# Performance work log

Measured on AMD Instinct MI355X. Metric: run time of the kernel, lower is better.

The kernel has to match this reference:

```python
import jax, jax.numpy as jnp
import numpy as np

B, N, K = 16, 2048, 20
EPS = 1e-5
SLOPE = 0.2  # LeakyReLU negative slope


def _lrelu(x):
    return jnp.where(x >= 0, x, SLOPE * x)


def _bn(x, g, b, axes):
    # BatchNorm in training mode (batch statistics), channel-last layout
    m = x.mean(axes, keepdims=True)
    v = x.var(axes, keepdims=True)
    return (x - m) * jax.lax.rsqrt(v + EPS) * g + b


def _graph_features(pts, k):
    # pts: [B, N, C] -> edge features [B, N, k, 2C] = concat(x_j - x_i, x_i)
    xx = jnp.sum(pts * pts, axis=-1)                       # [B, N]
    inner = jnp.einsum('bnc,bmc->bnm', pts, pts)           # [B, N, N]
    neg_d = 2.0 * inner - xx[:, :, None] - xx[:, None, :]  # -||x_i - x_j||^2
    _, idx = jax.lax.top_k(neg_d, k)                       # [B, N, k]
    xj = jax.vmap(lambda p, i: p[i])(pts, idx)             # [B, N, k, C]
    xi = pts[:, :, None, :]                                # [B, N, 1, C]
    return jnp.concatenate([xj - xi, jnp.broadcast_to(xi, xj.shape)], axis=-1)


def _forward(x, conv_w, conv_g, conv_b, w1, b1, g1, bt1, w2, b2, g2, bt2,
             w3, b3, g3, bt3, w4, b4, w5, b5):
    feat = _graph_features(x, K)                           # [B, N, K, 6]
    # 1x1 Conv2d (bias=False) + BN2d + LeakyReLU, then max over neighbors
    h = jnp.einsum('bnkc,oc->bnko', feat, conv_w)          # [B, N, K, 64]
    h = _lrelu(_bn(h, conv_g, conv_b, (0, 1, 2)))
    h = h.max(axis=2)                                      # [B, N, 64]
    # DBR blocks: Linear + BN1d + LeakyReLU over points
    h = _lrelu(_bn(h @ w1 + b1, g1, bt1, (0, 1)))          # [B, N, 64]
    h = _lrelu(_bn(h @ w2 + b2, g2, bt2, (0, 1)))          # [B, N, 128]
    h = _lrelu(_bn(h @ w3 + b3, g3, bt3, (0, 1)))          # [B, N, 128]
    h = h.max(axis=1)                                      # MaxChannel -> [B, 128]
    h = _lrelu(h @ w4 + b4)                                # DbR -> [B, 512]
    return h @ w5 + b5                                     # [B, 2*Z_DIM=256]


def setup_inputs() -> dict:
    key = jax.random.key(0)
    ks = jax.random.split(key, 8)
    rn = lambda k, s, sc: (jax.random.normal(k, s, jnp.float32) * sc)
    return {
        'x': jax.random.normal(ks[0], (B, N, 3), jnp.float32),
        'conv_w': rn(ks[1], (64, 6), 0.3),
        'conv_g': jnp.ones(64, jnp.float32), 'conv_b': jnp.zeros(64, jnp.float32),
        'w1': rn(ks[2], (64, 64), 0.1), 'b1': jnp.zeros(64, jnp.float32),
        'g1': jnp.ones(64, jnp.float32), 'bt1': jnp.zeros(64, jnp.float32),
        'w2': rn(ks[3], (64, 128), 0.1), 'b2': jnp.zeros(128, jnp.float32),
        'g2': jnp.ones(128, jnp.float32), 'bt2': jnp.zeros(128, jnp.float32),
        'w3': rn(ks[4], (128, 128), 0.1), 'b3': jnp.zeros(128, jnp.float32),
        'g3': jnp.ones(128, jnp.float32), 'bt3': jnp.zeros(128, jnp.float32),
        'w4': rn(ks[5], (128, 512), 0.05), 'b4': jnp.zeros(512, jnp.float32),
        'w5': rn(ks[6], (512, 256), 0.05), 'b5': jnp.zeros(256, jnp.float32),
    }


def reference(x, conv_w, conv_g, conv_b, w1, b1, g1, bt1, w2, b2, g2, bt2,
              w3, b3, g3, bt3, w4, b4, w5, b5):
    return _forward(x, conv_w, conv_g, conv_b, w1, b1, g1, bt1, w2, b2, g2, bt2,
                    w3, b3, g3, bt3, w4, b4, w5, b5)
```

## Files before the change

### kernel.cpp

```cpp
#include <hip/hip_runtime.h>
#include <math.h>

#define NB   16
#define NPTS 2048
#define KNBR 20
#define NROWS (NB*NPTS)
#define CONV_M ((double)(NB)*(double)(NPTS)*(double)(KNBR))
#define ROW_M  ((double)NROWS)
#define BN_EPS 1e-5
#define LSLOPE 0.2f

__device__ __forceinline__ float lrelu(float v) { return v >= 0.f ? v : LSLOPE * v; }

__device__ __forceinline__ float4 stage4(float px, float py, float pz)
{
    return make_float4(px + px, py + py, pz + pz,
                       -fmaf(px, px, fmaf(py, py, pz * pz)));
}

__device__ __forceinline__ float dist_eval(float4 q, float4 c)
{
    float t = fmaf(c.x, q.x, fmaf(c.y, q.y, fmaf(c.z, q.z, q.w)));
    return t + c.w;
}

__device__ __forceinline__ void pair_insert_sorted(float (&bestv)[KNBR], float t0, float t1)
{
#pragma unroll
    for (int j = 0; j < KNBR; ++j) {
        float bj = bestv[j];
        float nb  = fmaxf(bj, t0);
        float nt0 = __builtin_amdgcn_fmed3f(bj, t0, t1);
        float nt1 = fminf(bj, t1);
        bestv[j] = nb;
        t0 = nt0; t1 = nt1;
    }
}

__global__ __launch_bounds__(256) void knn_feat_kernel(const float* __restrict__ x,
        const float* __restrict__ conv_w,
        float* __restrict__ maxh, float* __restrict__ minh, double* __restrict__ S)
{
    __shared__ float4 pts[NPTS];
    __shared__ unsigned short idxl[32][KNBR];
    __shared__ float  featw[4][KNBR][6];
    __shared__ double sred[4][27];
    __shared__ float  tbuf[32];
    const int b  = blockIdx.x >> 6;
    const int qg = blockIdx.x & 63;
    const float* xb = x + (size_t)b * NPTS * 3;
    for (int i = threadIdx.x; i < NPTS; i += 256)
        pts[i] = stage4(xb[i*3+0], xb[i*3+1], xb[i*3+2]);
    __syncthreads();

    {
        const int qi = threadIdx.x >> 3;
        const int c  = threadIdx.x & 7;
        const int n  = qg * 32 + qi;
        const float4 qc = pts[n];
        const float4 q = make_float4(0.5f*qc.x, 0.5f*qc.y, 0.5f*qc.z, qc.w);
        const int cbase = c * 256;
        const int rot   = (37 * c) & 255;
        float bestv[KNBR];
#pragma unroll
        for (int j = 0; j < KNBR; ++j) bestv[j] = -__builtin_inff();
        for (int m = 0; m < 64; m += 2) {
            const int j0 = (m + rot) & 255;
            const int j1 = (j0 + 1) & 255;
            float d0 = dist_eval(q, pts[cbase + j0]);
            float d1 = dist_eval(q, pts[cbase + j1]);
            pair_insert_sorted(bestv, fmaxf(d0, d1), fminf(d0, d1));
        }
        float L = bestv[KNBR-1];
        L = fmaxf(L, __shfl_xor(L, 1));
        L = fmaxf(L, __shfl_xor(L, 2));
        L = fmaxf(L, __shfl_xor(L, 4));
#pragma unroll
        for (int j = 0; j < KNBR; ++j) bestv[j] = fmaxf(bestv[j], L);
        float thresh = bestv[KNBR-1];
        float r0 = -__builtin_inff(), r1 = r0, r2 = r0, r3 = r0;
        int rc = 0;
        for (int m = 64; m < 256; m += 2) {
            const int j0 = (m + rot) & 255;
            const int j1 = (j0 + 1) & 255;
            float d0 = dist_eval(q, pts[cbase + j0]);
            float d1 = dist_eval(q, pts[cbase + j1]);
            bool h0 = d0 > thresh;
            r3 = h0 ? r2 : r3; r2 = h0 ? r1 : r2; r1 = h0 ? r0 : r1; r0 = h0 ? d0 : r0;
            rc += h0 ? 1 : 0;
            bool h1 = d1 > thresh;
            r3 = h1 ? r2 : r3; r2 = h1 ? r1 : r2; r1 = h1 ? r0 : r1; r0 = h1 ? d1 : r0;
            rc += h1 ? 1 : 0;
            if (__any(rc >= 3)) {
                pair_insert_sorted(bestv, fmaxf(r0, r1), fminf(r0, r1));
                pair_insert_sorted(bestv, fmaxf(r2, r3), fminf(r2, r3));
                r0 = r1 = r2 = r3 = -__builtin_inff();
                rc = 0;
                thresh = bestv[KNBR-1];
            }
        }
        pair_insert_sorted(bestv, fmaxf(r0, r1), fminf(r0, r1));
        pair_insert_sorted(bestv, fmaxf(r2, r3), fminf(r2, r3));
#pragma unroll
        for (int lev = 1; lev <= 4; lev <<= 1) {
            float orig[KNBR];
#pragma unroll
            for (int j = 0; j < KNBR; ++j) orig[j] = bestv[j];
            for (int i = 0; i < KNBR; i += 2) {
                float nb0 = __shfl_xor(orig[i],   lev);
                float nb1 = __shfl_xor(orig[i+1], lev);
                if (!__any(nb0 > bestv[KNBR-1])) break;
                pair_insert_sorted(bestv, nb0, nb1);
            }
        }
        if (c == 0) tbuf[qi] = bestv[KNBR-1];
    }
    __syncthreads();

    const int wv = threadIdx.x >> 6, lane = threadIdx.x & 63;
    const unsigned long long below = (1ull << lane) - 1ull;
    for (int qi2 = 0; qi2 < 8; ++qi2) {
        const int p = wv * 8 + qi2;
        const int n = qg * 32 + p;
        const float4 qc = pts[n];
        const float4 q = make_float4(0.5f*qc.x, 0.5f*qc.y, 0.5f*qc.z, qc.w);
        const float th = tbuf[p];
        int cnt = 0;
        for (int it = 0; it < 32; ++it) {
            float d = dist_eval(q, pts[it*64 + lane]);
            const bool hit = (d >= th);
            unsigned long long mask = __ballot(hit);
            int pos = cnt + __popcll(mask & below);
            if (hit && pos < KNBR)
                idxl[p][pos] = (unsigned short)(it*64 + lane);
            cnt += __popcll(mask);
        }
    }
    __syncthreads();

    float cw[6];
#pragma unroll
    for (int c = 0; c < 6; ++c) cw[c] = conv_w[lane*6 + c];
    int pa_ = 0, pb_ = 0;
    if (lane >= 6 && lane < 27) {
        int t = lane - 6, a = 0;
        while (t >= 6 - a) { t -= 6 - a; ++a; }
        pa_ = a; pb_ = a + t;
    }
    double acc = 0.0;
    for (int i = 0; i < 8; ++i) {
        const int p = wv * 8 + i;
        const int nn = qg * 32 + p;
        const size_t bp = (size_t)b * NPTS + nn;
        const float4 Ci = pts[nn];
        const float xi0 = 0.5f*Ci.x, xi1 = 0.5f*Ci.y, xi2 = 0.5f*Ci.z;
        float f0=0,f1=0,f2=0,f3=0,f4=0,f5=0;
        if (lane < KNBR) {
            const float4 Cj = pts[idxl[p][lane]];
            f0 = 0.5f*(Cj.x - Ci.x);
            f1 = 0.5f*(Cj.y - Ci.y);
            f2 = 0.5f*(Cj.z - Ci.z);
            f3 = xi0; f4 = xi1; f5 = xi2;
        }
        __syncthreads();
        if (lane < KNBR) {
            featw[wv][lane][0]=f0; featw[wv][lane][1]=f1; featw[wv][lane][2]=f2;
            featw[wv][lane][3]=f3; featw[wv][lane][4]=f4; featw[wv][lane][5]=f5;
        }
        __syncthreads();
        float vmax = -__builtin_inff(), vmin = __builtin_inff();
#pragma unroll
        for (int k = 0; k < KNBR; ++k) {
            float h = featw[wv][k][0] * cw[0];
            h = fmaf(featw[wv][k][1], cw[1], h);
            h = fmaf(featw[wv][k][2], cw[2], h);
            h = fmaf(featw[wv][k][3], cw[3], h);
            h = fmaf(featw[wv][k][4], cw[4], h);
            h = fmaf(featw[wv][k][5], cw[5], h);
            vmax = fmaxf(vmax, h); vmin = fminf(vmin, h);
        }
        maxh[bp*64 + lane] = vmax;
        minh[bp*64 + lane] = vmin;
        if (lane < 6) {
            double s = 0;
#pragma unroll
            for (int k = 0; k < KNBR; ++k) s += (double)featw[wv][k][lane];
            acc += s;
        } else if (lane < 27) {
            double s = 0;
#pragma unroll
            for (int k = 0; k < KNBR; ++k)
                s += (double)featw[wv][k][pa_] * (double)featw[wv][k][pb_];
            acc += s;
        }
    }
    if (lane < 27) sred[wv][lane] = acc;
    __syncthreads();
    if (threadIdx.x < 27) {
        double tot = sred[0][threadIdx.x] + sred[1][threadIdx.x]
                   + sred[2][threadIdx.x] + sred[3][threadIdx.x];
        atomicAdd(&S[threadIdx.x], tot);
    }
}

template<int K, int N, bool SEL, bool POOLOUT, bool STATS0>
__global__ __launch_bounds__(256) void mlp_gemm(const float* __restrict__ A,
        const float* __restrict__ A2,
        const double* __restrict__ st_a, const double* __restrict__ st_b,
        const float* __restrict__ st_g, const float* __restrict__ st_bt,
        const float* __restrict__ cwm,
        const float* __restrict__ W, const float* __restrict__ bias,
        float* __restrict__ Y, double* __restrict__ sum, double* __restrict__ sq,
        float* __restrict__ pmax_g, float* __restrict__ pmin_g)
{
    constexpr int CPT = N / 16;
    __shared__ float As[64 * 64];
    __shared__ float Ws[64 * N];
    __shared__ __align__(16) float s_scale[K], s_shift[K];
    const int tid = threadIdx.x;
    if (tid < K) {
        const int o = tid;
        if (STATS0) {
            double w[6];
#pragma unroll
            for (int c = 0; c < 6; ++c) w[c] = (double)cwm[o*6 + c];
            double mean = 0.0;
#pragma unroll
            for (int c = 0; c < 6; ++c) mean += w[c] * st_a[c];
            mean /= CONV_M;
            double ey2 = 0.0;
            int t = 6;
#pragma unroll
            for (int a = 0; a < 6; ++a)
#pragma unroll
                for (int b2 = a; b2 < 6; ++b2) {
                    double coef = (a == b2) ? 1.0 : 2.0;
                    ey2 += coef * w[a] * w[b2] * st_a[t];
                    ++t;
                }
            ey2 /= CONV_M;
            double var = ey2 - mean * mean;
            double sc = (double)st_g[o] / sqrt(var + BN_EPS);
            s_scale[o] = (float)sc;
            s_shift[o] = (float)((double)st_bt[o] - mean * sc);
        } else {
            double m = st_a[o] / ROW_M;
            double v = st_b[o] / ROW_M - m * m;
            double sc = (double)st_g[o] / sqrt(v + BN_EPS);
            s_scale[o] = (float)sc;
            s_shift[o] = (float)((double)st_bt[o] - m * sc);
        }
    }
    const int row0 = blockIdx.x * 64;
    const int ct = tid & 15, rt = tid >> 4;
    float acc[4][CPT];
#pragma unroll
    for (int rr = 0; rr < 4; ++rr)
#pragma unroll
        for (int cc = 0; cc < CPT; ++cc) acc[rr][cc] = bias[ct*CPT + cc];
    __syncthreads();

    for (int kk = 0; kk < K/64; ++kk) {
        if (kk) __syncthreads();
#pragma unroll
        for (int i = 0; i < 4; ++i) {
            const int f   = i * 256 + tid;
            const int k4  = f & 15;
            const int row = f >> 4;
            const int kg  = kk*64 + k4*4;
            float4 m = *(const float4*)(A + (size_t)(row0+row)*K + kg);
            const float4 s4 = *(const float4*)(&s_scale[kg]);
            const float4 h4 = *(const float4*)(&s_shift[kg]);
            if (SEL) {
                float4 m2 = *(const float4*)(A2 + (size_t)(row0+row)*K + kg);
                m.x = s4.x >= 0.f ? m.x : m2.x;
                m.y = s4.y >= 0.f ? m.y : m2.y;
                m.z = s4.z >= 0.f ? m.z : m2.z;
                m.w = s4.w >= 0.f ? m.w : m2.w;
            }
            const int rsw = row ^ ((k4 & 7) << 2);
            As[(k4*4+0)*64 + rsw] = lrelu(fmaf(s4.x, m.x, h4.x));
            As[(k4*4+1)*64 + rsw] = lrelu(fmaf(s4.y, m.y, h4.y));
            As[(k4*4+2)*64 + rsw] = lrelu(fmaf(s4.z, m.z, h4.z));
            As[(k4*4+3)*64 + rsw] = lrelu(fmaf(s4.w, m.w, h4.w));
        }
#pragma unroll
        for (int i = 0; i < N/16; ++i) {
            const int f    = i * 256 + tid;
            const int col4 = f & (N/4 - 1);
            const int krow = f / (N/4);
            *(float4*)(&Ws[krow*N + col4*4]) =
                *(const float4*)(W + (size_t)(kk*64 + krow)*N + col4*4);
        }
        __syncthreads();
#pragma unroll 4
        for (int k = 0; k < 64; ++k) {
            const int sw = ((k >> 2) & 7) << 2;
            const float4 a0 = *(const float4*)(&As[k*64 + ((rt*4) ^ sw)]);
            float a_[4] = {a0.x, a0.y, a0.z, a0.w};
            float w_[CPT];
#pragma unroll
            for (int v = 0; v < CPT/4; ++v) {
                const float4 wv4 = *(const float4*)(&Ws[k*N + ct*CPT + v*4]);
                w_[v*4+0] = wv4.x; w_[v*4+1] = wv4.y; w_[v*4+2] = wv4.z; w_[v*4+3] = wv4.w;
            }
#pragma unroll
            for (int rr = 0; rr < 4; ++rr)
#pragma unroll
                for (int cc = 0; cc < CPT; ++cc)
                    acc[rr][cc] = fmaf(a_[rr], w_[cc], acc[rr][cc]);
        }
    }
    if (!POOLOUT) {
#pragma unroll
        for (int rr = 0; rr < 4; ++rr) {
            float* yo = Y + (size_t)(row0 + rt*4 + rr)*N + ct*CPT;
#pragma unroll
            for (int v = 0; v < CPT/4; ++v)
                *(float4*)(yo + v*4) = make_float4(acc[rr][v*4+0], acc[rr][v*4+1],
                                                   acc[rr][v*4+2], acc[rr][v*4+3]);
        }
    }
    __syncthreads();
    float* cr  = As;
    float* pmx = As + 512;
    float* pmn = Ws;
    if (tid < 2*N) cr[tid] = 0.f;
    if (POOLOUT) {
#pragma unroll
        for (int cc = 0; cc < CPT; ++cc) {
            float vmax = fmaxf(fmaxf(acc[0][cc], acc[1][cc]), fmaxf(acc[2][cc], acc[3][cc]));
            float vmin = fminf(fminf(acc[0][cc], acc[1][cc]), fminf(acc[2][cc], acc[3][cc]));
            pmx[rt*N + ct*CPT + cc] = vmax;
            pmn[rt*N + ct*CPT + cc] = vmin;
        }
    }
    __syncthreads();
#pragma unroll
    for (int cc = 0; cc < CPT; ++cc) {
        float s = acc[0][cc] + acc[1][cc] + acc[2][cc] + acc[3][cc];
        float q = fmaf(acc[0][cc], acc[0][cc], 0.f);
        q = fmaf(acc[1][cc], acc[1][cc], q);
        q = fmaf(acc[2][cc], acc[2][cc], q);
        q = fmaf(acc[3][cc], acc[3][cc], q);
        atomicAdd(&cr[ct*CPT + cc], s);
        atomicAdd(&cr[N + ct*CPT + cc], q);
    }
    float rm = 0.f, rn = 0.f;
    if (POOLOUT && tid < N) {
        rm = pmx[tid]; rn = pmn[tid];
#pragma unroll
        for (int r = 1; r < 16; ++r) {
            rm = fmaxf(rm, pmx[r*N + tid]);
            rn = fminf(rn, pmn[r*N + tid]);
        }
    }
    __syncthreads();
    if (tid < N) {
        atomicAdd(&sum[tid], (double)cr[tid]);
        atomicAdd(&sq[tid],  (double)cr[N + tid]);
        if (POOLOUT) {
            pmax_g[(size_t)blockIdx.x * N + tid] = rm;
            pmin_g[(size_t)blockIdx.x * N + tid] = rn;
        }
    }
}

__global__ __launch_bounds__(256) void headpool_kernel(const float* __restrict__ pmax_g,
        const float* __restrict__ pmin_g,
        const double* __restrict__ sum3, const double* __restrict__ sq3,
        const float* __restrict__ g3, const float* __restrict__ bt3,
        const float* __restrict__ w4, const float* __restrict__ b4,
        const float* __restrict__ w5, const float* __restrict__ b5,
        float* __restrict__ out)
{
    __shared__ float xr[128];
    __shared__ float hh[512];
    const int b = blockIdx.x, t = threadIdx.x;
    if (t < 128) {
        double m_ = sum3[t] / ROW_M;
        double v_ = sq3[t] / ROW_M - m_ * m_;
        double scd = (double)g3[t] / sqrt(v_ + BN_EPS);
        const float sc = (float)scd;
        const float sh = (float)((double)bt3[t] - m_ * scd);
        const float* pm = pmax_g + (size_t)b * 32 * 128 + t;
        const float* pn = pmin_g + (size_t)b * 32 * 128 + t;
        float m = pm[0], n_ = pn[0];
#pragma unroll
        for (int r = 1; r < 32; ++r) {
            m  = fmaxf(m,  pm[r*128]);
            n_ = fminf(n_, pn[r*128]);
        }
        xr[t] = lrelu(sc >= 0.f ? fmaf(sc, m, sh) : fmaf(sc, n_, sh));
    }
    __syncthreads();
    float h0 = b4[t], h1 = b4[t + 256];
    for (int c = 0; c < 128; ++c) {
        float xc = xr[c];
        h0 = fmaf(xc, w4[c*512 + t],       h0);
        h1 = fmaf(xc, w4[c*512 + t + 256], h1);
    }
    hh[t]       = lrelu(h0);
    hh[t + 256] = lrelu(h1);
    __syncthreads();
    float acc = b5[t];
    for (int c = 0; c < 512; ++c)
        acc = fmaf(hh[c], w5[c*256 + t], acc);
    out[b*256 + t] = acc;
}

extern "C" void kernel_launch(void* const* d_in, const int* in_sizes, int n_in,
                              void* d_out, int out_size, void* d_ws, size_t ws_size,
                              hipStream_t stream)
{
    const float* x      = (const float*)d_in[0];
    const float* conv_w = (const float*)d_in[1];
    const float* conv_g = (const float*)d_in[2];
    const float* conv_b = (const float*)d_in[3];
    const float* w1  = (const float*)d_in[4];
    const float* b1  = (const float*)d_in[5];
    const float* g1  = (const float*)d_in[6];
    const float* bt1 = (const float*)d_in[7];
    const float* w2  = (const float*)d_in[8];
    const float* b2  = (const float*)d_in[9];
    const float* g2  = (const float*)d_in[10];
    const float* bt2 = (const float*)d_in[11];
    const float* w3  = (const float*)d_in[12];
    const float* b3  = (const float*)d_in[13];
    const float* g3  = (const float*)d_in[14];
    const float* bt3 = (const float*)d_in[15];
    const float* w4  = (const float*)d_in[16];
    const float* b4  = (const float*)d_in[17];
    const float* w5  = (const float*)d_in[18];
    const float* b5  = (const float*)d_in[19];

    char* p = (char*)d_ws;
    auto take = [&](size_t bytes) -> char* {
        char* r = p; p += (bytes + 255) & ~(size_t)255; return r;
    };
    double* S    = (double*)take(27 * 8);
    double* sum1 = (double*)take(64 * 8);
    double* sq1  = (double*)take(64 * 8);
    double* sum2 = (double*)take(128 * 8);
    double* sq2  = (double*)take(128 * 8);
    double* sum3 = (double*)take(128 * 8);
    double* sq3  = (double*)take(128 * 8);
    size_t zero_bytes = (size_t)(p - (char*)d_ws);
    float* pmaxg  = (float*)take((size_t)512 * 128 * 4);
    float* pming  = (float*)take((size_t)512 * 128 * 4);
    float* mm     = (float*)take((size_t)NROWS * 128 * 4);
    float* maxh   = mm;
    float* minh   = mm + (size_t)NROWS * 64;
    float* y1     = (float*)take((size_t)NROWS * 64 * 4);
    float* y2     = (float*)take((size_t)NROWS * 128 * 4);

    hipMemsetAsync(d_ws, 0, zero_bytes, stream);
    knn_feat_kernel<<<dim3(NB * 64), dim3(256), 0, stream>>>(x, conv_w, maxh, minh, S);

    mlp_gemm<64,64,true,false,true>    <<<dim3(512), dim3(256), 0, stream>>>(
        maxh, minh, S, nullptr, conv_g, conv_b, conv_w, w1, b1, y1, sum1, sq1, nullptr, nullptr);
    mlp_gemm<64,128,false,false,false> <<<dim3(512), dim3(256), 0, stream>>>(
        y1, y1, sum1, sq1, g1, bt1, nullptr, w2, b2, y2, sum2, sq2, nullptr, nullptr);
    mlp_gemm<128,128,false,true,false> <<<dim3(512), dim3(256), 0, stream>>>(
        y2, y2, sum2, sq2, g2, bt2, nullptr, w3, b3, nullptr, sum3, sq3, pmaxg, pming);

    headpool_kernel<<<dim3(NB), dim3(256), 0, stream>>>(
        pmaxg, pming, sum3, sq3, g3, bt3, w4, b4, w5, b5, (float*)d_out);
}
```

Before: 342.8 us.

## Replace per-lane kNN insertion with sampled bound plus wave-wide bisection select

Each of the 8 lanes per query now scans only 64 points instead of 256. The merged top-20 of this 512-point sample gives a lower bound on the true 20th-largest score. A full wave pass then stores the distances at or above that bound in shared memory (up to 120). A 32-step bisection over order-preserving integer keys, using ballots, finds the exact 20th value. A final pass writes the indices. Two block barriers are dropped because each wave only uses its own queries' data. The cost is two extra full distance sweeps. If more than 120 candidates pass the bound, a slow fallback rescans all points on every bisection step.

```diff
diff --git a/kernel.cpp b/kernel.cpp
--- a/kernel.cpp
+++ b/kernel.cpp
@@ -4,6 +4,7 @@
 #define NB   16
 #define NPTS 2048
 #define KNBR 20
+#define SCAP 120
 #define NROWS (NB*NPTS)
 #define CONV_M ((double)(NB)*(double)(NPTS)*(double)(KNBR))
 #define ROW_M  ((double)NROWS)
@@ -37,17 +38,31 @@
     }
 }
 
+__device__ __forceinline__ unsigned omap(float f)
+{
+    unsigned b = __float_as_uint(f);
+    return b ^ (unsigned)(((int)b >> 31) | (int)0x80000000);
+}
+__device__ __forceinline__ float ounmap(unsigned u)
+{
+    unsigned b = (u & 0x80000000u) ? (u ^ 0x80000000u) : ~u;
+    return __uint_as_float(b);
+}
+
 __global__ __launch_bounds__(256) void knn_feat_kernel(const float* __restrict__ x,
         const float* __restrict__ conv_w,
         float* __restrict__ maxh, float* __restrict__ minh, double* __restrict__ S)
 {
     __shared__ float4 pts[NPTS];
+    __shared__ float  sval[32][SCAP];
+    __shared__ float  tbuf[32];
+    __shared__ int    scnt[32];
     __shared__ unsigned short idxl[32][KNBR];
     __shared__ float  featw[4][KNBR][6];
     __shared__ double sred[4][27];
-    __shared__ float  tbuf[32];
     const int b  = blockIdx.x >> 6;
     const int qg = blockIdx.x & 63;
+    const int wv = threadIdx.x >> 6, lane = threadIdx.x & 63;
     const float* xb = x + (size_t)b * NPTS * 3;
     for (int i = threadIdx.x; i < NPTS; i += 256)
         pts[i] = stage4(xb[i*3+0], xb[i*3+1], xb[i*3+2]);
@@ -59,48 +74,16 @@
         const int n  = qg * 32 + qi;
         const float4 qc = pts[n];
         const float4 q = make_float4(0.5f*qc.x, 0.5f*qc.y, 0.5f*qc.z, qc.w);
-        const int cbase = c * 256;
-        const int rot   = (37 * c) & 255;
         float bestv[KNBR];
 #pragma unroll
         for (int j = 0; j < KNBR; ++j) bestv[j] = -__builtin_inff();
         for (int m = 0; m < 64; m += 2) {
-            const int j0 = (m + rot) & 255;
-            const int j1 = (j0 + 1) & 255;
-            float d0 = dist_eval(q, pts[cbase + j0]);
-            float d1 = dist_eval(q, pts[cbase + j1]);
+            const int j0 = c*64 + ((m + c) & 63);
+            const int j1 = c*64 + ((m + 1 + c) & 63);
+            float d0 = dist_eval(q, pts[j0]);
+            float d1 = dist_eval(q, pts[j1]);
             pair_insert_sorted(bestv, fmaxf(d0, d1), fminf(d0, d1));
         }
-        float L = bestv[KNBR-1];
-        L = fmaxf(L, __shfl_xor(L, 1));
-        L = fmaxf(L, __shfl_xor(L, 2));
-        L = fmaxf(L, __shfl_xor(L, 4));
-#pragma unroll
-        for (int j = 0; j < KNBR; ++j) bestv[j] = fmaxf(bestv[j], L);
-        float thresh = bestv[KNBR-1];
-        float r0 = -__builtin_inff(), r1 = r0, r2 = r0, r3 = r0;
-        int rc = 0;
-        for (int m = 64; m < 256; m += 2) {
-            const int j0 = (m + rot) & 255;
-            const int j1 = (j0 + 1) & 255;
-            float d0 = dist_eval(q, pts[cbase + j0]);
-            float d1 = dist_eval(q, pts[cbase + j1]);
-            bool h0 = d0 > thresh;
-            r3 = h0 ? r2 : r3; r2 = h0 ? r1 : r2; r1 = h0 ? r0 : r1; r0 = h0 ? d0 : r0;
-            rc += h0 ? 1 : 0;
-            bool h1 = d1 > thresh;
-            r3 = h1 ? r2 : r3; r2 = h1 ? r1 : r2; r1 = h1 ? r0 : r1; r0 = h1 ? d1 : r0;
-            rc += h1 ? 1 : 0;
-            if (__any(rc >= 3)) {
-                pair_insert_sorted(bestv, fmaxf(r0, r1), fminf(r0, r1));
-                pair_insert_sorted(bestv, fmaxf(r2, r3), fminf(r2, r3));
-                r0 = r1 = r2 = r3 = -__builtin_inff();
-                rc = 0;
-                thresh = bestv[KNBR-1];
-            }
-        }
-        pair_insert_sorted(bestv, fmaxf(r0, r1), fminf(r0, r1));
-        pair_insert_sorted(bestv, fmaxf(r2, r3), fminf(r2, r3));
 #pragma unroll
         for (int lev = 1; lev <= 4; lev <<= 1) {
             float orig[KNBR];
@@ -115,28 +98,63 @@
         }
         if (c == 0) tbuf[qi] = bestv[KNBR-1];
     }
-    __syncthreads();
-
-    const int wv = threadIdx.x >> 6, lane = threadIdx.x & 63;
+
     const unsigned long long below = (1ull << lane) - 1ull;
     for (int qi2 = 0; qi2 < 8; ++qi2) {
         const int p = wv * 8 + qi2;
         const int n = qg * 32 + p;
         const float4 qc = pts[n];
         const float4 q = make_float4(0.5f*qc.x, 0.5f*qc.y, 0.5f*qc.z, qc.w);
-        const float th = tbuf[p];
+        const float L = tbuf[p];
         int cnt = 0;
         for (int it = 0; it < 32; ++it) {
             float d = dist_eval(q, pts[it*64 + lane]);
-            const bool hit = (d >= th);
+            const bool hit = (d >= L);
             unsigned long long mask = __ballot(hit);
             int pos = cnt + __popcll(mask & below);
+            if (hit && pos < SCAP) sval[p][pos] = d;
+            cnt += __popcll(mask);
+        }
+        float thresh;
+        if (cnt <= SCAP) {
+            unsigned u0 = (lane      < cnt) ? omap(sval[p][lane])      : 0u;
+            unsigned u1 = (lane + 64 < cnt) ? omap(sval[p][lane + 64]) : 0u;
+            unsigned lo = 0u, hi = 0xFFFFFFFFu;
+#pragma unroll
+            for (int s = 0; s < 32; ++s) {
+                unsigned mid = lo + ((hi - lo) >> 1);
+                int c2 = __popcll(__ballot(u0 >= mid)) + __popcll(__ballot(u1 >= mid));
+                bool ge = (c2 >= KNBR);
+                lo = ge ? mid : lo;
+                hi = ge ? hi : mid;
+            }
+            thresh = ounmap(lo);
+        } else {
+            unsigned lo = 0u, hi = 0xFFFFFFFFu;
+            for (int s = 0; s < 32; ++s) {
+                unsigned mid = lo + ((hi - lo) >> 1);
+                int c2 = 0;
+                for (int it = 0; it < 32; ++it) {
+                    float d = dist_eval(q, pts[it*64 + lane]);
+                    c2 += __popcll(__ballot(omap(d) >= mid));
+                }
+                bool ge = (c2 >= KNBR);
+                lo = ge ? mid : lo;
+                hi = ge ? hi : mid;
+            }
+            thresh = ounmap(lo);
+        }
+        int cnt2 = 0;
+        for (int it = 0; it < 32; ++it) {
+            float d = dist_eval(q, pts[it*64 + lane]);
+            const bool hit = (d >= thresh);
+            unsigned long long mask = __ballot(hit);
+            int pos = cnt2 + __popcll(mask & below);
             if (hit && pos < KNBR)
                 idxl[p][pos] = (unsigned short)(it*64 + lane);
-            cnt += __popcll(mask);
-        }
-    }
-    __syncthreads();
+            cnt2 += __popcll(mask);
+        }
+    }
 
     float cw[6];
 #pragma unroll
```

Result: slower. 417.7 us (+21.8%).
